# Performance work log

Hardware: AMD Instinct MI355X
Metric: run time of the kernel (lower is better)

The kernel has to match this reference:

```python
import jax, jax.numpy as jnp
import numpy as np

N_HEAD = 16
D_HEAD = 64
D_MODEL = 1024
LN_EPS = 1e-5


def layer_norm(x, gamma, beta):
    mu = jnp.mean(x, axis=-1, keepdims=True)
    var = jnp.mean((x - mu) ** 2, axis=-1, keepdims=True)
    return (x - mu) * jax.lax.rsqrt(var + LN_EPS) * gamma + beta


def setup_inputs() -> dict:
    key = jax.random.key(0)
    ks = jax.random.split(key, 6)
    B, T = 2, 2048
    inp = jax.random.normal(ks[0], (B, T, D_MODEL), dtype=jnp.float32)
    # qkv_net: Linear(d_model, 3*n_head*d_head)
    W_qkv = jax.random.normal(ks[1], (3 * N_HEAD * D_HEAD, D_MODEL), dtype=jnp.float32) * (D_MODEL ** -0.5)
    b_qkv = jax.random.normal(ks[2], (3 * N_HEAD * D_HEAD,), dtype=jnp.float32) * 0.02
    # o_net: Linear(n_head*d_head, d_model, bias=False)
    W_o = jax.random.normal(ks[3], (D_MODEL, N_HEAD * D_HEAD), dtype=jnp.float32) * ((N_HEAD * D_HEAD) ** -0.5)
    gamma = jnp.ones((D_MODEL,), dtype=jnp.float32)
    beta = jnp.zeros((D_MODEL,), dtype=jnp.float32)
    return {"inp": inp, "W_qkv": W_qkv, "b_qkv": b_qkv, "W_o": W_o, "gamma": gamma, "beta": beta}


def reference(inp, W_qkv, b_qkv, W_o, gamma, beta):
    B, T, D = inp.shape
    H, dh = N_HEAD, D_HEAD
    scale = 1.0 / (dh ** 0.5)

    qkv = inp @ W_qkv.T + b_qkv                      # (B, T, 3*H*dh)
    head_q, head_k, head_v = jnp.split(qkv, 3, axis=2)
    # (B, T, H, dh) -> (B, H, T, dh)
    q = head_q.reshape(B, T, H, dh).transpose(0, 2, 1, 3)
    k = head_k.reshape(B, T, H, dh).transpose(0, 2, 1, 3)
    v = head_v.reshape(B, T, H, dh).transpose(0, 2, 1, 3)

    attn_score = jnp.einsum('bhqd,bhkd->bhqk', q, k) * scale  # (B, H, T, T)
    attn_prob = jax.nn.softmax(attn_score, axis=-1)           # dropatt is identity in eval
    attn_vec = jnp.einsum('bhqk,bhkd->bhqd', attn_prob, v)    # (B, H, T, dh)

    # Faithful to original: (B*H, T, dh) batch-major buffer is VIEWED as (H, B, T, dh)
    attn_vec = attn_vec.reshape(H, B, T, dh)
    attn_vec = attn_vec.transpose(1, 2, 0, 3).reshape(B, T, H * dh)

    attn_out = attn_vec @ W_o.T                                # dropout identity in eval
    return layer_norm(inp + attn_out, gamma, beta)
```

## Files before the change

kernel.cpp:

```cpp
#include <hip/hip_runtime.h>
#include <hip/hip_bf16.h>
#include <stdint.h>

typedef __bf16 bf16_t;
typedef __bf16 bf16x8 __attribute__((ext_vector_type(8)));
typedef __bf16 bf16x4 __attribute__((ext_vector_type(4)));
typedef float floatx4 __attribute__((ext_vector_type(4)));

#define QSCALE 0.180336879f

__device__ static inline void gll16(const void* g, void* l) {
    __builtin_amdgcn_global_load_lds((const __attribute__((address_space(1))) void*)g,
                                     (__attribute__((address_space(3))) void*)l, 16, 0, 0);
}

__global__ __launch_bounds__(256) void cvt_all(const float* __restrict__ inp,
                                               const float* __restrict__ wqkv,
                                               const float* __restrict__ wo,
                                               bf16_t* __restrict__ o_inp,
                                               bf16_t* __restrict__ o_wqkv,
                                               bf16_t* __restrict__ o_wo) {
    int blk = blockIdx.x;
    const float* src;
    bf16_t* dst;
    if (blk < 4096)      { src = inp;  dst = o_inp; }
    else if (blk < 7168) { src = wqkv; dst = o_wqkv; blk -= 4096; }
    else                 { src = wo;   dst = o_wo;   blk -= 7168; }
    int i = blk * 256 + threadIdx.x;
    float4 v = ((const float4*)src)[i];
    bf16x4 o;
    o[0] = (bf16_t)v.x; o[1] = (bf16_t)v.y; o[2] = (bf16_t)v.z; o[3] = (bf16_t)v.w;
    ((bf16x4*)dst)[i] = o;
}

__global__ __launch_bounds__(256, 3)
void gemm_qkv(const bf16_t* __restrict__ A, const bf16_t* __restrict__ Bw,
              const float* __restrict__ bias,
              bf16_t* __restrict__ qk, bf16_t* __restrict__ vT) {
    constexpr int K = 1024;
    __shared__ bf16_t lA[128 * 32];
    __shared__ bf16_t lB[128 * 32];
    const int tid  = threadIdx.x;
    const int lane = tid & 63, wave = tid >> 6;
    const int quad = lane >> 4, l16 = lane & 15;
    const int wy = wave >> 1, wx = wave & 1;
    const int bm = blockIdx.y * 128, bn = blockIdx.x * 128;

    const int c0 = tid, c1 = tid + 256;
    const bf16_t* Ap0 = A + (size_t)(bm + (c0 >> 2)) * K + (c0 & 3) * 8;
    const bf16_t* Ap1 = A + (size_t)(bm + (c1 >> 2)) * K + (c1 & 3) * 8;
    const bf16_t* Bp0 = Bw + (size_t)(bn + (c0 >> 2)) * K + (c0 & 3) * 8;
    const bf16_t* Bp1 = Bw + (size_t)(bn + (c1 >> 2)) * K + (c1 & 3) * 8;
    bf16_t* dA0 = &lA[(wave * 64) * 8];
    bf16_t* dA1 = &lA[(256 + wave * 64) * 8];
    bf16_t* dB0 = &lB[(wave * 64) * 8];
    bf16_t* dB1 = &lB[(256 + wave * 64) * 8];

    floatx4 acc[4][4] = {};

    for (int kt = 0; kt < K; kt += 32) {
        __syncthreads();
        gll16(Ap0 + kt, dA0);
        gll16(Ap1 + kt, dA1);
        gll16(Bp0 + kt, dB0);
        gll16(Bp1 + kt, dB1);
        __syncthreads();
        bf16x8 af[4], bfr[4];
#pragma unroll
        for (int i = 0; i < 4; i++) {
            af[i]  = *(const bf16x8*)(lA + (wy * 64 + i * 16 + l16) * 32 + quad * 8);
            bfr[i] = *(const bf16x8*)(lB + (wx * 64 + i * 16 + l16) * 32 + quad * 8);
        }
#pragma unroll
        for (int i = 0; i < 4; i++)
#pragma unroll
            for (int j = 0; j < 4; j++)
                acc[i][j] = __builtin_amdgcn_mfma_f32_16x16x32_bf16(af[i], bfr[j], acc[i][j], 0, 0, 0);
    }

    const bool is_v = (bn >= 2048);
#pragma unroll
    for (int j = 0; j < 4; j++) {
        const int n = bn + wx * 64 + j * 16 + l16;
        const float bv = bias[n];
        const bool isq = (n < 1024);
#pragma unroll
        for (int i = 0; i < 4; i++) {
            const int mbase = bm + wy * 64 + i * 16 + quad * 4;
            if (!is_v) {
#pragma unroll
                for (int r = 0; r < 4; r++) {
                    float c = acc[i][j][r] + bv;
                    if (isq) c *= QSCALE;
                    qk[(size_t)(mbase + r) * 2048 + n] = (bf16_t)c;
                }
            } else {
                const int nn = n - 2048;
                const int b  = mbase >> 11;
                const int t  = mbase & 2047;
                const int vrow = b * 1024 + nn;
                bf16x4 pack;
#pragma unroll
                for (int r = 0; r < 4; r++) pack[r] = (bf16_t)(acc[i][j][r] + bv);
                *(bf16x4*)(vT + (size_t)vrow * 2048 + t) = pack;
            }
        }
    }
}

__global__ __launch_bounds__(256, 4)
void attn_kernel(const bf16_t* __restrict__ qk, const bf16_t* __restrict__ vT,
                 bf16_t* __restrict__ Opart, float* __restrict__ lpart) {
    __shared__ bf16_t Kbuf[2][64 * 64];
    __shared__ bf16_t Vbuf[2][64 * 64];
    __shared__ bf16_t Pbuf[4][16 * 32];
    const int tid  = threadIdx.x;
    const int lane = tid & 63, wave = tid >> 6;
    const int quad = lane >> 4, l16 = lane & 15;
    const int bid = blockIdx.x;
    const int s    = bid & 63;
    const int hl   = ((s & 7) << 2) | ((s >> 3) & 3);
    const int half = (s >> 5) & 1;
    const int qt   = bid >> 6;
    const int b = hl >> 4, h = hl & 15;
    const int kt0 = half * 1024;

    const bf16_t* Qbase = qk + (size_t)(b * 2048 + qt * 128 + wave * 32) * 2048 + h * 64;
    const bf16_t* Kbase = qk + (size_t)(b * 2048) * 2048 + 1024 + h * 64;
    const bf16_t* Vbase = vT + (size_t)(hl * 64) * 2048;

    const int srow = tid >> 2, sc8 = (tid & 3) * 8;
    const bf16_t* KgA = Kbase + (size_t)(kt0 + srow) * 2048 + sc8;
    const bf16_t* KgB = KgA + 32;
    const bf16_t* VgA = Vbase + (size_t)srow * 2048 + kt0 + sc8;
    const bf16_t* VgB = VgA + 32;
    const int wbase = wave * 512;

    bf16x8 qf[2][2];
#pragma unroll
    for (int rt = 0; rt < 2; rt++)
#pragma unroll
        for (int kc = 0; kc < 2; kc++)
            qf[rt][kc] = *(const bf16x8*)(Qbase + (size_t)(rt * 16 + l16) * 2048 + kc * 32 + quad * 8);

    floatx4 accO[2][4] = {};
    float lacc[2] = {0.f, 0.f};

    gll16(KgA, &Kbuf[0][wbase]);
    gll16(KgB, &Kbuf[0][2048 + wbase]);
    gll16(VgA, &Vbuf[0][wbase]);
    gll16(VgB, &Vbuf[0][2048 + wbase]);

    for (int it = 0; it < 16; ++it) {
        const int cur = it & 1, nxt = cur ^ 1;
        __syncthreads();
        if (it < 15) {
            const size_t ko = (size_t)(it + 1) * 64 * 2048;
            const int    vo = (it + 1) * 64;
            gll16(KgA + ko, &Kbuf[nxt][wbase]);
            gll16(KgB + ko, &Kbuf[nxt][2048 + wbase]);
            gll16(VgA + vo, &Vbuf[nxt][wbase]);
            gll16(VgB + vo, &Vbuf[nxt][2048 + wbase]);
        }
        floatx4 st[2][4] = {};
#pragma unroll
        for (int nt = 0; nt < 4; nt++) {
            bf16x8 k0 = *(const bf16x8*)&Kbuf[cur][(nt * 16 + l16) * 32 + quad * 8];
            bf16x8 k1 = *(const bf16x8*)&Kbuf[cur][2048 + (nt * 16 + l16) * 32 + quad * 8];
            st[0][nt] = __builtin_amdgcn_mfma_f32_16x16x32_bf16(k0, qf[0][0], st[0][nt], 0, 0, 0);
            st[0][nt] = __builtin_amdgcn_mfma_f32_16x16x32_bf16(k1, qf[0][1], st[0][nt], 0, 0, 0);
            st[1][nt] = __builtin_amdgcn_mfma_f32_16x16x32_bf16(k0, qf[1][0], st[1][nt], 0, 0, 0);
            st[1][nt] = __builtin_amdgcn_mfma_f32_16x16x32_bf16(k1, qf[1][1], st[1][nt], 0, 0, 0);
        }
#pragma unroll
        for (int kc2 = 0; kc2 < 2; kc2++) {
            bf16x8 vf[4];
#pragma unroll
            for (int ct = 0; ct < 4; ct++)
                vf[ct] = *(const bf16x8*)&Vbuf[cur][kc2 * 2048 + (ct * 16 + l16) * 32 + quad * 8];
#pragma unroll
            for (int rt = 0; rt < 2; rt++) {
                float ls = 0.f;
#pragma unroll
                for (int ntl = 0; ntl < 2; ntl++) {
                    const floatx4 sv = st[rt][kc2 * 2 + ntl];
                    bf16x4 pk;
#pragma unroll
                    for (int r = 0; r < 4; r++) {
                        float p = __builtin_amdgcn_exp2f(sv[r]);
                        ls += p;
                        pk[r] = (bf16_t)p;
                    }
                    *(bf16x4*)&Pbuf[wave][l16 * 32 + ntl * 16 + quad * 4] = pk;
                }
                lacc[rt] += ls;
                bf16x8 pf = *(const bf16x8*)&Pbuf[wave][l16 * 32 + quad * 8];
#pragma unroll
                for (int ct = 0; ct < 4; ct++)
                    accO[rt][ct] = __builtin_amdgcn_mfma_f32_16x16x32_bf16(pf, vf[ct], accO[rt][ct], 0, 0, 0);
            }
        }
    }

    float lsum[2];
#pragma unroll
    for (int rt = 0; rt < 2; rt++) {
        float l = lacc[rt];
        l += __shfl_xor(l, 16);
        l += __shfl_xor(l, 32);
        lsum[rt] = l;
    }
    const int b2 = hl & 1;
    const int colb = hl >> 1;
    const int rowb = b2 * 2048 + qt * 128 + wave * 32;
    bf16_t* outb = Opart + (size_t)half * (4096 * 1024) + (size_t)rowb * 1024 + colb * 64;
#pragma unroll
    for (int rt = 0; rt < 2; rt++)
#pragma unroll
        for (int ct = 0; ct < 4; ct++)
#pragma unroll
            for (int r = 0; r < 4; r++)
                outb[(size_t)(rt * 16 + quad * 4 + r) * 1024 + ct * 16 + l16] = (bf16_t)(accO[rt][ct][r]);
    if (quad == 0) {
#pragma unroll
        for (int rt = 0; rt < 2; rt++)
            lpart[half * 65536 + (rowb + rt * 16 + l16) * 16 + colb] = lsum[rt];
    }
}

__global__ __launch_bounds__(256)
void attn_combine(const bf16_t* __restrict__ Op, const float* __restrict__ lp,
                  bf16_t* __restrict__ av) {
    const int row = blockIdx.x, tid = threadIdx.x;
    const int col = tid * 4, cb = col >> 6;
    const float l = lp[row * 16 + cb] + lp[65536 + row * 16 + cb];
    const float inv = 1.0f / l;
    bf16x4 o0 = *(const bf16x4*)(Op + (size_t)row * 1024 + col);
    bf16x4 o1 = *(const bf16x4*)(Op + (size_t)(4096 + row) * 1024 + col);
    bf16x4 o;
#pragma unroll
    for (int i = 0; i < 4; i++)
        o[i] = (bf16_t)(((float)o0[i] + (float)o1[i]) * inv);
    *(bf16x4*)(av + (size_t)row * 1024 + col) = o;
}

__global__ __launch_bounds__(256, 4)
void gemm_o(const bf16_t* __restrict__ A, const bf16_t* __restrict__ Bw,
            float* __restrict__ out) {
    constexpr int K = 1024;
    __shared__ bf16_t lA[64 * 32];
    __shared__ bf16_t lB[128 * 32];
    const int tid  = threadIdx.x;
    const int lane = tid & 63, wave = tid >> 6;
    const int quad = lane >> 4, l16 = lane & 15;
    const int wy = wave >> 1, wx = wave & 1;
    const int bm = blockIdx.y * 64, bn = blockIdx.x * 128;

    const int ca = tid;
    const int cb0 = tid, cb1 = tid + 256;
    const bf16_t* Ap  = A + (size_t)(bm + (ca >> 2)) * K + (ca & 3) * 8;
    const bf16_t* Bp0 = Bw + (size_t)(bn + (cb0 >> 2)) * K + (cb0 & 3) * 8;
    const bf16_t* Bp1 = Bw + (size_t)(bn + (cb1 >> 2)) * K + (cb1 & 3) * 8;
    bf16_t* dA  = &lA[(wave * 64) * 8];
    bf16_t* dB0 = &lB[(wave * 64) * 8];
    bf16_t* dB1 = &lB[(256 + wave * 64) * 8];

    floatx4 acc[2][4] = {};
    for (int kt = 0; kt < K; kt += 32) {
        __syncthreads();
        gll16(Ap + kt, dA);
        gll16(Bp0 + kt, dB0);
        gll16(Bp1 + kt, dB1);
        __syncthreads();
        bf16x8 af[2], bfr[4];
#pragma unroll
        for (int i = 0; i < 2; i++)
            af[i] = *(const bf16x8*)(lA + (wy * 32 + i * 16 + l16) * 32 + quad * 8);
#pragma unroll
        for (int j = 0; j < 4; j++)
            bfr[j] = *(const bf16x8*)(lB + (wx * 64 + j * 16 + l16) * 32 + quad * 8);
#pragma unroll
        for (int i = 0; i < 2; i++)
#pragma unroll
            for (int j = 0; j < 4; j++)
                acc[i][j] = __builtin_amdgcn_mfma_f32_16x16x32_bf16(af[i], bfr[j], acc[i][j], 0, 0, 0);
    }
#pragma unroll
    for (int j = 0; j < 4; j++) {
        const int n = bn + wx * 64 + j * 16 + l16;
#pragma unroll
        for (int i = 0; i < 2; i++) {
            const int mbase = bm + wy * 32 + i * 16 + quad * 4;
#pragma unroll
            for (int r = 0; r < 4; r++)
                out[(size_t)(mbase + r) * 1024 + n] = acc[i][j][r];
        }
    }
}

__global__ __launch_bounds__(256)
void ln_kernel(const float* __restrict__ inp, const float* __restrict__ ao,
               const float* __restrict__ gamma, const float* __restrict__ beta,
               float* __restrict__ out) {
    const int row = blockIdx.x, tid = threadIdx.x;
    const int wave = tid >> 6, lane = tid & 63;
    float4 a = ((const float4*)(inp + (size_t)row * 1024))[tid];
    float4 c = ((const float4*)(ao + (size_t)row * 1024))[tid];
    float x0 = a.x + c.x, x1 = a.y + c.y, x2 = a.z + c.z, x3 = a.w + c.w;
    float s = x0 + x1 + x2 + x3;
    float sq = x0 * x0 + x1 * x1 + x2 * x2 + x3 * x3;
#pragma unroll
    for (int mm = 32; mm >= 1; mm >>= 1) {
        s += __shfl_xor(s, mm);
        sq += __shfl_xor(sq, mm);
    }
    __shared__ float rs[4], rq[4];
    if (lane == 0) { rs[wave] = s; rq[wave] = sq; }
    __syncthreads();
    s = rs[0] + rs[1] + rs[2] + rs[3];
    sq = rq[0] + rq[1] + rq[2] + rq[3];
    const float mu = s * (1.0f / 1024.0f);
    const float var = sq * (1.0f / 1024.0f) - mu * mu;
    const float rstd = rsqrtf(var + 1e-5f);
    float4 g = ((const float4*)gamma)[tid], bt = ((const float4*)beta)[tid];
    float4 o;
    o.x = (x0 - mu) * rstd * g.x + bt.x;
    o.y = (x1 - mu) * rstd * g.y + bt.y;
    o.z = (x2 - mu) * rstd * g.z + bt.z;
    o.w = (x3 - mu) * rstd * g.w + bt.w;
    ((float4*)(out + (size_t)row * 1024))[tid] = o;
}

extern "C" void kernel_launch(void* const* d_in, const int* in_sizes, int n_in,
                              void* d_out, int out_size, void* d_ws, size_t ws_size,
                              hipStream_t stream) {
    const float* inp   = (const float*)d_in[0];
    const float* Wqkv  = (const float*)d_in[1];
    const float* bqkv  = (const float*)d_in[2];
    const float* Wo    = (const float*)d_in[3];
    const float* gamma = (const float*)d_in[4];
    const float* beta  = (const float*)d_in[5];
    float* out = (float*)d_out;

    char* ws = (char*)d_ws;
    bf16_t* inp_bf  = (bf16_t*)(ws);
    bf16_t* wqkv_bf = (bf16_t*)(ws + (8u << 20));
    bf16_t* wo_bf   = (bf16_t*)(ws + (14u << 20));
    bf16_t* qk_buf  = (bf16_t*)(ws + (16u << 20));
    bf16_t* vT_buf  = (bf16_t*)(ws + (32u << 20));
    bf16_t* av_buf  = (bf16_t*)(ws + (40u << 20));
    float*  ao_buf  = (float*)(ws + (48u << 20));
    bf16_t* opart   = (bf16_t*)(ws + (48u << 20));
    float*  lpart   = (float*)(ws);

    cvt_all<<<8192, 256, 0, stream>>>(inp, Wqkv, Wo, inp_bf, wqkv_bf, wo_bf);
    gemm_qkv<<<dim3(24, 32), 256, 0, stream>>>(inp_bf, wqkv_bf, bqkv, qk_buf, vT_buf);
    attn_kernel<<<1024, 256, 0, stream>>>(qk_buf, vT_buf, opart, lpart);
    attn_combine<<<4096, 256, 0, stream>>>(opart, lpart, av_buf);
    gemm_o<<<dim3(8, 64), 256, 0, stream>>>(av_buf, wo_bf, ao_buf);
    ln_kernel<<<4096, 256, 0, stream>>>(inp, ao_buf, gamma, beta, out);
}
```

Before: 216.0 us.

## Keep P in registers via permuted V layout and fuse split-K combine into gemm_o

The QKV GEMM now writes V^T with a permuted column order inside each 32-key block, so the softmax probabilities from the QK^T accumulator can feed the PV MFMA straight from registers. This removes the per-wave LDS round-trip through Pbuf. The separate attn_combine kernel is also removed: gemm_o now loads both partial outputs, divides by the summed row normalisers and writes the A tile to LDS itself. This saves a launch and an intermediate buffer write and read, but the A operand now uses plain register loads instead of async global-to-LDS loads, and the B loads overlap less with them.

```diff
diff --git a/kernel.cpp b/kernel.cpp
--- a/kernel.cpp
+++ b/kernel.cpp
@@ -99,10 +99,11 @@
                 const int b  = mbase >> 11;
                 const int t  = mbase & 2047;
                 const int vrow = b * 1024 + nn;
+                const int pcol = (t & ~31) | (((t >> 2) & 3) << 3) | (((t >> 4) & 1) << 2);
                 bf16x4 pack;
 #pragma unroll
                 for (int r = 0; r < 4; r++) pack[r] = (bf16_t)(acc[i][j][r] + bv);
-                *(bf16x4*)(vT + (size_t)vrow * 2048 + t) = pack;
+                *(bf16x4*)(vT + (size_t)vrow * 2048 + pcol) = pack;
             }
         }
     }
@@ -113,7 +114,6 @@
                  bf16_t* __restrict__ Opart, float* __restrict__ lpart) {
     __shared__ bf16_t Kbuf[2][64 * 64];
     __shared__ bf16_t Vbuf[2][64 * 64];
-    __shared__ bf16_t Pbuf[4][16 * 32];
     const int tid  = threadIdx.x;
     const int lane = tid & 63, wave = tid >> 6;
     const int quad = lane >> 4, l16 = lane & 15;
@@ -180,21 +180,15 @@
                 vf[ct] = *(const bf16x8*)&Vbuf[cur][kc2 * 2048 + (ct * 16 + l16) * 32 + quad * 8];
 #pragma unroll
             for (int rt = 0; rt < 2; rt++) {
+                bf16x8 pf;
                 float ls = 0.f;
 #pragma unroll
-                for (int ntl = 0; ntl < 2; ntl++) {
-                    const floatx4 sv = st[rt][kc2 * 2 + ntl];
-                    bf16x4 pk;
-#pragma unroll
-                    for (int r = 0; r < 4; r++) {
-                        float p = __builtin_amdgcn_exp2f(sv[r]);
-                        ls += p;
-                        pk[r] = (bf16_t)p;
-                    }
-                    *(bf16x4*)&Pbuf[wave][l16 * 32 + ntl * 16 + quad * 4] = pk;
+                for (int j = 0; j < 8; j++) {
+                    float p = __builtin_amdgcn_exp2f(st[rt][kc2 * 2 + (j >> 2)][j & 3]);
+                    ls += p;
+                    pf[j] = (bf16_t)p;
                 }
                 lacc[rt] += ls;
-                bf16x8 pf = *(const bf16x8*)&Pbuf[wave][l16 * 32 + quad * 8];
 #pragma unroll
                 for (int ct = 0; ct < 4; ct++)
                     accO[rt][ct] = __builtin_amdgcn_mfma_f32_16x16x32_bf16(pf, vf[ct], accO[rt][ct], 0, 0, 0);
@@ -228,25 +222,9 @@
     }
 }
 
-__global__ __launch_bounds__(256)
-void attn_combine(const bf16_t* __restrict__ Op, const float* __restrict__ lp,
-                  bf16_t* __restrict__ av) {
-    const int row = blockIdx.x, tid = threadIdx.x;
-    const int col = tid * 4, cb = col >> 6;
-    const float l = lp[row * 16 + cb] + lp[65536 + row * 16 + cb];
-    const float inv = 1.0f / l;
-    bf16x4 o0 = *(const bf16x4*)(Op + (size_t)row * 1024 + col);
-    bf16x4 o1 = *(const bf16x4*)(Op + (size_t)(4096 + row) * 1024 + col);
-    bf16x4 o;
-#pragma unroll
-    for (int i = 0; i < 4; i++)
-        o[i] = (bf16_t)(((float)o0[i] + (float)o1[i]) * inv);
-    *(bf16x4*)(av + (size_t)row * 1024 + col) = o;
-}
-
 __global__ __launch_bounds__(256, 4)
-void gemm_o(const bf16_t* __restrict__ A, const bf16_t* __restrict__ Bw,
-            float* __restrict__ out) {
+void gemm_o(const bf16_t* __restrict__ Op, const float* __restrict__ lp,
+            const bf16_t* __restrict__ Bw, float* __restrict__ out) {
     constexpr int K = 1024;
     __shared__ bf16_t lA[64 * 32];
     __shared__ bf16_t lB[128 * 32];
@@ -257,20 +235,31 @@
     const int bm = blockIdx.y * 64, bn = blockIdx.x * 128;
 
     const int ca = tid;
+    const int arow = bm + (ca >> 2);
+    const int ak   = (ca & 3) * 8;
+    const bf16_t* Ap0 = Op + (size_t)arow * 1024 + ak;
+    const bf16_t* Ap1 = Ap0 + (size_t)4096 * 1024;
+    const float*  lrow = lp + arow * 16;
     const int cb0 = tid, cb1 = tid + 256;
-    const bf16_t* Ap  = A + (size_t)(bm + (ca >> 2)) * K + (ca & 3) * 8;
     const bf16_t* Bp0 = Bw + (size_t)(bn + (cb0 >> 2)) * K + (cb0 & 3) * 8;
     const bf16_t* Bp1 = Bw + (size_t)(bn + (cb1 >> 2)) * K + (cb1 & 3) * 8;
-    bf16_t* dA  = &lA[(wave * 64) * 8];
     bf16_t* dB0 = &lB[(wave * 64) * 8];
     bf16_t* dB1 = &lB[(256 + wave * 64) * 8];
 
     floatx4 acc[2][4] = {};
     for (int kt = 0; kt < K; kt += 32) {
-        __syncthreads();
-        gll16(Ap + kt, dA);
+        bf16x8 a0 = *(const bf16x8*)(Ap0 + kt);
+        bf16x8 a1 = *(const bf16x8*)(Ap1 + kt);
+        const int cb = (kt + ak) >> 6;
+        const float inv = 1.0f / (lrow[cb] + lrow[65536 + cb]);
+        bf16x8 av;
+#pragma unroll
+        for (int j = 0; j < 8; j++)
+            av[j] = (bf16_t)(((float)a0[j] + (float)a1[j]) * inv);
+        __syncthreads();
         gll16(Bp0 + kt, dB0);
         gll16(Bp1 + kt, dB1);
+        *(bf16x8*)&lA[ca * 8] = av;
         __syncthreads();
         bf16x8 af[2], bfr[4];
 #pragma unroll
@@ -348,15 +337,13 @@
     bf16_t* wo_bf   = (bf16_t*)(ws + (14u << 20));
     bf16_t* qk_buf  = (bf16_t*)(ws + (16u << 20));
     bf16_t* vT_buf  = (bf16_t*)(ws + (32u << 20));
-    bf16_t* av_buf  = (bf16_t*)(ws + (40u << 20));
-    float*  ao_buf  = (float*)(ws + (48u << 20));
+    float*  ao_buf  = (float*)(ws + (32u << 20));
     bf16_t* opart   = (bf16_t*)(ws + (48u << 20));
     float*  lpart   = (float*)(ws);
 
     cvt_all<<<8192, 256, 0, stream>>>(inp, Wqkv, Wo, inp_bf, wqkv_bf, wo_bf);
     gemm_qkv<<<dim3(24, 32), 256, 0, stream>>>(inp_bf, wqkv_bf, bqkv, qk_buf, vT_buf);
     attn_kernel<<<1024, 256, 0, stream>>>(qk_buf, vT_buf, opart, lpart);
-    attn_combine<<<4096, 256, 0, stream>>>(opart, lpart, av_buf);
-    gemm_o<<<dim3(8, 64), 256, 0, stream>>>(av_buf, wo_bf, ao_buf);
+    gemm_o<<<dim3(8, 64), 256, 0, stream>>>(opart, lpart, wo_bf, ao_buf);
     ln_kernel<<<4096, 256, 0, stream>>>(inp, ao_buf, gamma, beta, out);
 }
```

Result: faster. 204.2 us (-5.4%).
